# Performance work log

Measured on AMD Instinct MI355X. Metric: run time of the kernel, lower is better.

Reference implementation:

```python
import jax, jax.numpy as jnp
import numpy as np

B, XL, YL, D = 16, 2048, 2048, 1024

def setup_inputs() -> dict:
    key = jax.random.key(0)
    kx, ky, km, kw = jax.random.split(key, 4)
    x = jax.random.normal(kx, (B, XL, D), dtype=jnp.float32)
    y = jax.random.normal(ky, (B, YL, D), dtype=jnp.float32)
    # True == padding position (masked with -inf in the torch module)
    y_mask = jax.random.randint(km, (B, YL), 0, 2).astype(bool)
    # shared projection Linear(embed_dim, embed_dim); scale ~ 1/sqrt(D)
    W = jax.random.normal(kw, (D, D), dtype=jnp.float32) * (1.0 / np.sqrt(D))
    b = jnp.zeros((D,), dtype=jnp.float32)
    return {"x": x, "y": y, "y_mask": y_mask, "W": W, "b": b}

def reference(x, y, y_mask, W, b):
    # shared ReLU(Linear) projection applied to both x and y
    x_proj = jax.nn.relu(jnp.einsum('bxd,ed->bxe', x, W) + b)   # (B, XL, D)
    y_proj = jax.nn.relu(jnp.einsum('byd,ed->bye', y, W) + b)   # (B, YL, D)
    scores = jnp.einsum('bxd,byd->bxy', x_proj, y_proj)          # (B, XL, YL)
    scores = jnp.where(y_mask[:, None, :], -jnp.inf, scores)
    weights = jax.nn.softmax(scores, axis=2)
    contexts = jnp.einsum('bxy,byd->bxd', weights, y)            # (B, XL, D)
    return contexts
```

## Files before the change

kernel.cpp:

```cpp
#include <hip/hip_runtime.h>
#include <math.h>
#include <stdint.h>


typedef __attribute__((ext_vector_type(8))) _Float16 f16x8;
typedef __attribute__((ext_vector_type(4))) float f32x4;

__device__ __forceinline__ ushort h2u(_Float16 h) { return __builtin_bit_cast(ushort, h); }

__device__ __forceinline__ void ld16(const ushort* g, ushort* l) {
    __builtin_amdgcn_global_load_lds(
        (__attribute__((address_space(1))) void*)(g),
        (__attribute__((address_space(3))) void*)(l), 16, 0, 0);
}

template<int EPI, int MODE>
__global__ __launch_bounds__(256) void gemm128(
    const ushort* __restrict__ A, size_t zsA,
    const ushort* __restrict__ B, size_t zsB,
    const float* __restrict__ bias, const int* __restrict__ nyBuf,
    float* __restrict__ Cf, ushort* __restrict__ Chi, size_t zsC,
    int sdA, int sdB, int N, int T)
{
    __shared__ char ldsb[32768];

    const int gx = gridDim.x, gxy = gx * gridDim.y;
    const int total = gxy * gridDim.z;
    int hsw = blockIdx.z * gxy + blockIdx.y * gx + blockIdx.x;
    hsw = (hsw & 7) * (total >> 3) + (hsw >> 3);
    const int z = hsw / gxy;
    const int rem = hsw - z * gxy;
    const int by = rem / gx;
    const int bx = rem - by * gx;

    int NY = 0, NYPAD = 0;
    if constexpr (MODE != 0) { NY = nyBuf[2 * z]; NYPAD = nyBuf[2 * z + 1]; }
    if constexpr (MODE == 1) { if (by * 128 >= 2048 && by * 128 - 2048 >= NYPAD) return; }
    if constexpr (MODE == 2) { if (bx * 128 >= NYPAD) return; }
    if constexpr (MODE == 3) { T = NYPAD >> 6; }

    const int tid = threadIdx.x;
    const int lane = tid & 63;
    const int wv = tid >> 6;
    const int wm = (wv >> 1) * 64, wn = (wv & 1) * 64;
    const int m0 = by * 128, n0 = bx * 128;

    const int pl  = tid >> 3;
    const int ss  = (tid & 7) ^ (pl & 7);
    const int sr0 = 2 * pl + (ss >> 2);
    const int ske = (ss & 3) * 8;
    const int tb  = tid * 16;

    const ushort* gA0 = A + (size_t)z * zsA + (size_t)(m0 + sr0) * sdA + ske;
    const ushort* gA1 = gA0 + (size_t)64 * sdA;
    const ushort* gB0 = B + (size_t)z * zsB + (size_t)(n0 + sr0) * sdB + ske;
    const ushort* gB1 = gB0 + (size_t)64 * sdB;

    const int fr = lane & 15, fq = lane >> 4;
    const int sl = (((fr & 1) << 2) | fq) ^ ((fr >> 1) & 7);
    const int aoff = wm * 64 + (fr >> 1) * 128 + sl * 16;
    const int boff = 16384 + wn * 64 + (fr >> 1) * 128 + sl * 16;

    f32x4 acc[4][4];
    #pragma unroll
    for (int i = 0; i < 4; ++i)
        #pragma unroll
        for (int j = 0; j < 4; ++j)
            acc[i][j] = (f32x4){0.f, 0.f, 0.f, 0.f};

    for (int t = 0; t < T; ++t) {
        ld16(gA0,      (ushort*)(ldsb + tb));
        ld16(gA1,      (ushort*)(ldsb + 4096 + tb));
        ld16(gA0 + 32, (ushort*)(ldsb + 8192 + tb));
        ld16(gA1 + 32, (ushort*)(ldsb + 12288 + tb));
        ld16(gB0,      (ushort*)(ldsb + 16384 + tb));
        ld16(gB1,      (ushort*)(ldsb + 20480 + tb));
        ld16(gB0 + 32, (ushort*)(ldsb + 24576 + tb));
        ld16(gB1 + 32, (ushort*)(ldsb + 28672 + tb));
        gA0 += 64; gA1 += 64; gB0 += 64; gB1 += 64;
        __syncthreads();

        #pragma unroll
        for (int kk = 0; kk < 2; ++kk) {
            const char* p = ldsb + kk * 8192;
            f16x8 a[4], b[4];
            #pragma unroll
            for (int i = 0; i < 4; ++i) a[i] = *(const f16x8*)(p + aoff + i * 1024);
            #pragma unroll
            for (int j = 0; j < 4; ++j) b[j] = *(const f16x8*)(p + boff + j * 1024);
            #pragma unroll
            for (int i = 0; i < 4; ++i)
                #pragma unroll
                for (int j = 0; j < 4; ++j)
                    acc[i][j] = __builtin_amdgcn_mfma_f32_16x16x32_f16(a[i], b[j], acc[i][j], 0, 0, 0);
        }
        __syncthreads();
    }

    #pragma unroll
    for (int j = 0; j < 4; ++j) {
        const int col = n0 + wn + j * 16 + fr;
        float bb = 0.f;
        if constexpr (EPI == 1) bb = bias[col];
        #pragma unroll
        for (int i = 0; i < 4; ++i) {
            const int row = m0 + wm + i * 16 + fq * 4;
            #pragma unroll
            for (int r = 0; r < 4; ++r) {
                const float v = acc[i][j][r];
                const size_t idx = (size_t)z * zsC + (size_t)(row + r) * N + col;
                if constexpr (EPI == 0) {
                    Cf[idx] = v;
                } else if constexpr (EPI == 1) {
                    Chi[idx] = h2u((_Float16)fmaxf(v + bb, 0.f));
                } else {
                    Cf[idx] = (col >= NY) ? -INFINITY : v;
                }
            }
        }
    }
}

__global__ __launch_bounds__(256) void build_idx(const int* __restrict__ mask,
    int* __restrict__ idx, int* __restrict__ nyBuf)
{
    const int z = blockIdx.x;
    const int* mb = mask + (size_t)z * 2048;
    __shared__ int part[256];
    const int tid = threadIdx.x;
    int keep[8]; int c = 0;
    #pragma unroll
    for (int k = 0; k < 8; ++k) { keep[k] = (mb[tid * 8 + k] == 0); c += keep[k]; }
    part[tid] = c;
    for (int off = 1; off < 256; off <<= 1) {
        __syncthreads();
        const int v = (tid >= off) ? part[tid - off] : 0;
        __syncthreads();
        part[tid] += v;
    }
    __syncthreads();
    int pos = part[tid] - c;
    #pragma unroll
    for (int k = 0; k < 8; ++k)
        if (keep[k]) idx[(size_t)z * 2048 + (pos++)] = tid * 8 + k;
    if (tid == 255) {
        const int ny = part[255];
        int nyp = (ny + 127) & ~127;
        if (nyp < 256) nyp = 256;
        nyBuf[2 * z] = ny;
        nyBuf[2 * z + 1] = nyp;
    }
}

__global__ __launch_bounds__(256) void cvt_f16(const float* __restrict__ in,
    ushort* __restrict__ o, size_t sIn4, size_t sOut)
{
    const size_t z = blockIdx.z;
    const int i = blockIdx.x * 256 + threadIdx.x;
    const float4 v = reinterpret_cast<const float4*>(in)[z * sIn4 + i];
    ushort4 h;
    h.x = h2u((_Float16)v.x); h.y = h2u((_Float16)v.y);
    h.z = h2u((_Float16)v.z); h.w = h2u((_Float16)v.w);
    reinterpret_cast<ushort4*>(o + z * sOut)[i] = h;
}

__global__ __launch_bounds__(256) void gather_y(const float* __restrict__ y,
    const int* __restrict__ idx, const int* __restrict__ nyBuf,
    ushort* __restrict__ rH, ushort* __restrict__ tT,
    size_t sIn, size_t sR, size_t sT)
{
    __shared__ float tile[32][33];
    const size_t z = blockIdx.z;
    const int NY = nyBuf[2 * z], NYPAD = nyBuf[2 * z + 1];
    const int r0 = blockIdx.y * 32;
    if (r0 >= NYPAD) return;
    const int c0 = blockIdx.x * 32;
    const float* yb = y + z * sIn;
    const int* idxb = idx + z * 2048;
    const int tx = threadIdx.x & 31, ty = threadIdx.x >> 5;
    #pragma unroll
    for (int k = 0; k < 4; ++k) {
        const int i = r0 + ty + k * 8;
        float v = 0.f;
        if (i < NY) v = yb[(size_t)idxb[i] * 1024 + c0 + tx];
        tile[ty + k * 8][tx] = v;
        rH[z * sR + (size_t)i * 1024 + c0 + tx] = h2u((_Float16)v);
    }
    __syncthreads();
    #pragma unroll
    for (int k = 0; k < 4; ++k) {
        const int c = c0 + ty + k * 8;
        tT[z * sT + (size_t)c * 2048 + r0 + tx] = h2u((_Float16)tile[tx][ty + k * 8]);
    }
}

__global__ __launch_bounds__(256) void softmax_f16(const float* __restrict__ S,
    ushort* __restrict__ Wout, const int* __restrict__ nyBuf, size_t sS, size_t sW)
{
    const size_t row = blockIdx.x;
    const size_t b = row >> 11, r = row & 2047;
    const int nf4 = nyBuf[2 * b + 1] >> 2;
    const float4* p4 = reinterpret_cast<const float4*>(S + b * sS + r * 2048);
    ushort4* q4 = reinterpret_cast<ushort4*>(Wout + b * sW + r * 2048);
    const int tid = threadIdx.x;

    const float4 NEG = {-INFINITY, -INFINITY, -INFINITY, -INFINITY};
    float4 v0 = (tid < nf4) ? p4[tid] : NEG;
    float4 v1 = (tid + 256 < nf4) ? p4[tid + 256] : NEG;
    float m = fmaxf(fmaxf(fmaxf(v0.x, v0.y), fmaxf(v0.z, v0.w)),
                    fmaxf(fmaxf(v1.x, v1.y), fmaxf(v1.z, v1.w)));
    #pragma unroll
    for (int off = 32; off >= 1; off >>= 1)
        m = fmaxf(m, __shfl_xor(m, off));

    __shared__ float redm[4], reds[4];
    if ((tid & 63) == 0) redm[tid >> 6] = m;
    __syncthreads();
    m = fmaxf(fmaxf(redm[0], redm[1]), fmaxf(redm[2], redm[3]));

    float e[8];
    e[0] = __expf(v0.x - m); e[1] = __expf(v0.y - m);
    e[2] = __expf(v0.z - m); e[3] = __expf(v0.w - m);
    e[4] = __expf(v1.x - m); e[5] = __expf(v1.y - m);
    e[6] = __expf(v1.z - m); e[7] = __expf(v1.w - m);
    float s = ((e[0] + e[1]) + (e[2] + e[3])) + ((e[4] + e[5]) + (e[6] + e[7]));
    #pragma unroll
    for (int off = 32; off >= 1; off >>= 1)
        s += __shfl_xor(s, off);
    if ((tid & 63) == 0) reds[tid >> 6] = s;
    __syncthreads();
    s = reds[0] + reds[1] + reds[2] + reds[3];

    const float inv = 1.f / s;
    ushort4 o0, o1;
    o0.x = h2u((_Float16)(e[0] * inv)); o0.y = h2u((_Float16)(e[1] * inv));
    o0.z = h2u((_Float16)(e[2] * inv)); o0.w = h2u((_Float16)(e[3] * inv));
    o1.x = h2u((_Float16)(e[4] * inv)); o1.y = h2u((_Float16)(e[5] * inv));
    o1.z = h2u((_Float16)(e[6] * inv)); o1.w = h2u((_Float16)(e[7] * inv));
    if (tid < nf4) q4[tid] = o0;
    if (tid + 256 < nf4) q4[tid + 256] = o1;
}

extern "C" void kernel_launch(void* const* d_in, const int* in_sizes, int n_in,
                              void* d_out, int out_size, void* d_ws, size_t ws_size,
                              hipStream_t stream)
{
    const float* x    = (const float*)d_in[0];
    const float* y    = (const float*)d_in[1];
    const int* ymask  = (const int*)d_in[2];
    const float* W    = (const float*)d_in[3];
    const float* bias = (const float*)d_in[4];
    float* out = (float*)d_out;

    const size_t BD = 2097152;

    const size_t perBatch = 29360128ull;
    int G = 16;
    while (G > 1 && 4194304ull + (size_t)G * perBatch > ws_size) G >>= 1;

    uint8_t* wsb = (uint8_t*)d_ws;
    ushort* W16  = (ushort*)wsb;
    int* idxBuf  = (int*)(wsb + 2097152);
    int* nyBuf   = (int*)(wsb + 2097152 + 131072);
    uint8_t* r1  = wsb + 4194304;
    uint8_t* r2  = r1 + (size_t)G * 16777216;
    uint8_t* r3  = r2 + (size_t)G * 8388608;

    ushort* xyHi = (ushort*)r1;
    float*  sc   = (float*)r1;
    ushort* pHi  = (ushort*)r2;
    ushort* yT   = (ushort*)r3;

    cvt_f16<<<dim3(1024, 1, 1), dim3(256), 0, stream>>>(W, W16, 0, 0);
    build_idx<<<dim3(16), dim3(256), 0, stream>>>(ymask, idxBuf, nyBuf);

    for (int bs = 0; bs < 16; bs += G) {
        const float* xg = x + (size_t)bs * BD;
        const float* yg = y + (size_t)bs * BD;
        const int* nyB  = nyBuf + 2 * bs;

        cvt_f16<<<dim3(2048, 1, G), dim3(256), 0, stream>>>(
            xg, xyHi, BD / 4, 8388608);
        gather_y<<<dim3(32, 64, G), dim3(256), 0, stream>>>(
            yg, idxBuf + (size_t)bs * 2048, nyB,
            xyHi + BD, yT, BD, 8388608, BD);

        gemm128<1, 1><<<dim3(8, 32, G), dim3(256), 0, stream>>>(
            xyHi, 8388608, W16, 0,
            bias, nyB,
            nullptr, pHi, 4194304, 1024, 1024, 1024, 16);

        gemm128<2, 2><<<dim3(16, 16, G), dim3(256), 0, stream>>>(
            pHi, 4194304, pHi + BD, 4194304,
            nullptr, nyB,
            sc, nullptr, 4194304, 1024, 1024, 2048, 16);

        softmax_f16<<<dim3(G * 2048), dim3(256), 0, stream>>>(
            sc, pHi, nyB, 4194304, 4194304);

        gemm128<0, 3><<<dim3(8, 16, G), dim3(256), 0, stream>>>(
            pHi, 4194304, yT, 2097152,
            nullptr, nyB,
            out + (size_t)bs * BD, nullptr, BD, 2048, 2048, 1024, 16);
    }
}
```

Before: 503.4 us.

## Fuse fp32-to-fp16 conversion and y gather into projection GEMM A-loads

Adds a projg kernel that reads x and gathered y rows directly in fp32, converts them to fp16 in registers and writes them into swizzled LDS, while W tiles are staged with async global-to-LDS loads. This removes the separate cvt_f16 pass over x and the row-major fp16 copy of gathered y, saving a full write and re-read of the fp16 activations. In exchange, the GEMM A path now reads twice as many bytes per element (fp32) and relies on a software prefetch into registers, which may reduce overlap and raise register pressure.

```diff
diff --git a/kernel.cpp b/kernel.cpp
--- a/kernel.cpp
+++ b/kernel.cpp
@@ -14,15 +14,17 @@
         (__attribute__((address_space(3))) void*)(l), 16, 0, 0);
 }
 
-template<int EPI, int MODE>
-__global__ __launch_bounds__(256) void gemm128(
-    const ushort* __restrict__ A, size_t zsA,
-    const ushort* __restrict__ B, size_t zsB,
-    const float* __restrict__ bias, const int* __restrict__ nyBuf,
-    float* __restrict__ Cf, ushort* __restrict__ Chi, size_t zsC,
-    int sdA, int sdB, int N, int T)
-{
-    __shared__ char ldsb[32768];
+#define BAR()  { __builtin_amdgcn_s_barrier(); asm volatile("" ::: "memory"); }
+#define VMW0() asm volatile("s_waitcnt vmcnt(0)" ::: "memory");
+#define LGKM0() { asm volatile("s_waitcnt lgkmcnt(0)" ::: "memory"); __builtin_amdgcn_sched_barrier(0); }
+
+__global__ __launch_bounds__(256) void projg(
+    const float* __restrict__ X, const float* __restrict__ Y,
+    const int* __restrict__ idx, const int* __restrict__ nyBuf,
+    const ushort* __restrict__ Wm, const float* __restrict__ bias,
+    ushort* __restrict__ P, int T)
+{
+    __shared__ char ldsb[49152];
 
     const int gx = gridDim.x, gxy = gx * gridDim.y;
     const int total = gxy * gridDim.z;
@@ -33,9 +35,149 @@
     const int by = rem / gx;
     const int bx = rem - by * gx;
 
+    const int NY = nyBuf[2 * z], NYPAD = nyBuf[2 * z + 1];
+    const int m0 = by * 128, n0 = bx * 128;
+    if (m0 >= 2048 + NYPAD) return;
+
+    const int tid = threadIdx.x;
+    const int lane = tid & 63;
+    const int wv = tid >> 6;
+    const int wm = (wv >> 1) * 64, wn = (wv & 1) * 64;
+
+    const int ar = tid >> 1, akh = tid & 1;
+    const int gr = m0 + ar;
+    const float* asrc = nullptr;
+    if (gr < 2048) {
+        asrc = X + (size_t)z * 2097152 + (size_t)gr * 1024;
+    } else {
+        const int i = gr - 2048;
+        if (i < NY) asrc = Y + (size_t)z * 2097152 + (size_t)idx[(size_t)z * 2048 + i] * 1024;
+    }
+    const int ap = ar >> 1, asub = ar & 1;
+    char* awp = ldsb + akh * 8192 + ap * 128;
+    int awq[4];
+    #pragma unroll
+    for (int q = 0; q < 4; ++q) awq[q] = ((((asub << 2) | q) ^ (ap & 7)) << 4);
+
+    const int pl  = tid >> 3;
+    const int ss  = (tid & 7) ^ (pl & 7);
+    const int sr0 = 2 * pl + (ss >> 2);
+    const int ske = (ss & 3) * 8;
+    const int tb  = tid * 16;
+    const ushort* gB0 = Wm + (size_t)(n0 + sr0) * 1024 + ske;
+    const ushort* gB1 = gB0 + 65536;
+
+    const int fr = lane & 15, fq = lane >> 4;
+    const int sl = (((fr & 1) << 2) | fq) ^ ((fr >> 1) & 7);
+    const int aoff = wm * 64 + (fr >> 1) * 128 + sl * 16;
+    const int boff = wn * 64 + (fr >> 1) * 128 + sl * 16;
+
+    f32x4 acc[4][4];
+    #pragma unroll
+    for (int i = 0; i < 4; ++i)
+        #pragma unroll
+        for (int j = 0; j < 4; ++j)
+            acc[i][j] = (f32x4){0.f, 0.f, 0.f, 0.f};
+
+    float4 v[8];
+
+    auto issueA = [&](int t) {
+        if (asrc) {
+            const float4* s = reinterpret_cast<const float4*>(asrc + (size_t)t * 64 + akh * 32);
+            #pragma unroll
+            for (int u = 0; u < 8; ++u) v[u] = s[u];
+        } else {
+            #pragma unroll
+            for (int u = 0; u < 8; ++u) v[u] = (float4){0.f, 0.f, 0.f, 0.f};
+        }
+    };
+    auto stageB = [&](int t, int buf) {
+        const ushort* b0 = gB0 + t * 64;
+        const ushort* b1 = gB1 + t * 64;
+        ushort* d = (ushort*)(ldsb + 16384 + buf * 16384);
+        ld16(b0,      (ushort*)((char*)d + tb));
+        ld16(b1,      (ushort*)((char*)d + 4096 + tb));
+        ld16(b0 + 32, (ushort*)((char*)d + 8192 + tb));
+        ld16(b1 + 32, (ushort*)((char*)d + 12288 + tb));
+    };
+    auto writeA = [&]() {
+        #pragma unroll
+        for (int q = 0; q < 4; ++q) {
+            const float4 a_ = v[2 * q], b_ = v[2 * q + 1];
+            f16x8 h;
+            h[0] = (_Float16)a_.x; h[1] = (_Float16)a_.y;
+            h[2] = (_Float16)a_.z; h[3] = (_Float16)a_.w;
+            h[4] = (_Float16)b_.x; h[5] = (_Float16)b_.y;
+            h[6] = (_Float16)b_.z; h[7] = (_Float16)b_.w;
+            *reinterpret_cast<f16x8*>(awp + awq[q]) = h;
+        }
+    };
+    auto computeT = [&](int buf) {
+        #pragma unroll
+        for (int kk = 0; kk < 2; ++kk) {
+            const char* pa = ldsb + kk * 8192;
+            const char* pb = ldsb + 16384 + buf * 16384 + kk * 8192;
+            f16x8 a[4], b[4];
+            #pragma unroll
+            for (int i = 0; i < 4; ++i) a[i] = *(const f16x8*)(pa + aoff + i * 1024);
+            #pragma unroll
+            for (int j = 0; j < 4; ++j) b[j] = *(const f16x8*)(pb + boff + j * 1024);
+            #pragma unroll
+            for (int i = 0; i < 4; ++i)
+                #pragma unroll
+                for (int j = 0; j < 4; ++j)
+                    acc[i][j] = __builtin_amdgcn_mfma_f32_16x16x32_f16(a[i], b[j], acc[i][j], 0, 0, 0);
+        }
+    };
+
+    issueA(0); stageB(0, 0);
+    for (int t = 0; t < T; ++t) {
+        VMW0();
+        BAR();
+        writeA();
+        if (t + 1 < T) { issueA(t + 1); stageB(t + 1, (t + 1) & 1); }
+        LGKM0();
+        BAR();
+        computeT(t & 1);
+    }
+
+    #pragma unroll
+    for (int j = 0; j < 4; ++j) {
+        const int col = n0 + wn + j * 16 + fr;
+        const float bb = bias[col];
+        #pragma unroll
+        for (int i = 0; i < 4; ++i) {
+            const int row = m0 + wm + i * 16 + fq * 4;
+            #pragma unroll
+            for (int r = 0; r < 4; ++r) {
+                const size_t o = (size_t)z * 4194304 + (size_t)(row + r) * 1024 + col;
+                P[o] = h2u((_Float16)fmaxf(acc[i][j][r] + bb, 0.f));
+            }
+        }
+    }
+}
+
+template<int EPI, int MODE>
+__global__ __launch_bounds__(256) void gemm128(
+    const ushort* __restrict__ A, size_t zsA,
+    const ushort* __restrict__ B, size_t zsB,
+    const float* __restrict__ bias, const int* __restrict__ nyBuf,
+    float* __restrict__ Cf, ushort* __restrict__ Chi, size_t zsC,
+    int sdA, int sdB, int N, int T)
+{
+    __shared__ char ldsb[32768];
+
+    const int gx = gridDim.x, gxy = gx * gridDim.y;
+    const int total = gxy * gridDim.z;
+    int hsw = blockIdx.z * gxy + blockIdx.y * gx + blockIdx.x;
+    hsw = (hsw & 7) * (total >> 3) + (hsw >> 3);
+    const int z = hsw / gxy;
+    const int rem = hsw - z * gxy;
+    const int by = rem / gx;
+    const int bx = rem - by * gx;
+
     int NY = 0, NYPAD = 0;
     if constexpr (MODE != 0) { NY = nyBuf[2 * z]; NYPAD = nyBuf[2 * z + 1]; }
-    if constexpr (MODE == 1) { if (by * 128 >= 2048 && by * 128 - 2048 >= NYPAD) return; }
     if constexpr (MODE == 2) { if (bx * 128 >= NYPAD) return; }
     if constexpr (MODE == 3) { T = NYPAD >> 6; }
 
@@ -108,13 +250,13 @@
             #pragma unroll
             for (int r = 0; r < 4; ++r) {
                 const float v = acc[i][j][r];
-                const size_t idx = (size_t)z * zsC + (size_t)(row + r) * N + col;
+                const size_t o = (size_t)z * zsC + (size_t)(row + r) * N + col;
                 if constexpr (EPI == 0) {
-                    Cf[idx] = v;
+                    Cf[o] = v;
                 } else if constexpr (EPI == 1) {
-                    Chi[idx] = h2u((_Float16)fmaxf(v + bb, 0.f));
+                    Chi[o] = h2u((_Float16)fmaxf(v + bb, 0.f));
                 } else {
-                    Cf[idx] = (col >= NY) ? -INFINITY : v;
+                    Cf[o] = (col >= NY) ? -INFINITY : v;
                 }
             }
         }
@@ -153,21 +295,19 @@
 }
 
 __global__ __launch_bounds__(256) void cvt_f16(const float* __restrict__ in,
-    ushort* __restrict__ o, size_t sIn4, size_t sOut)
-{
-    const size_t z = blockIdx.z;
+    ushort* __restrict__ o)
+{
     const int i = blockIdx.x * 256 + threadIdx.x;
-    const float4 v = reinterpret_cast<const float4*>(in)[z * sIn4 + i];
+    const float4 v = reinterpret_cast<const float4*>(in)[i];
     ushort4 h;
     h.x = h2u((_Float16)v.x); h.y = h2u((_Float16)v.y);
     h.z = h2u((_Float16)v.z); h.w = h2u((_Float16)v.w);
-    reinterpret_cast<ushort4*>(o + z * sOut)[i] = h;
-}
-
-__global__ __launch_bounds__(256) void gather_y(const float* __restrict__ y,
+    reinterpret_cast<ushort4*>(o)[i] = h;
+}
+
+__global__ __launch_bounds__(256) void gather_t(const float* __restrict__ y,
     const int* __restrict__ idx, const int* __restrict__ nyBuf,
-    ushort* __restrict__ rH, ushort* __restrict__ tT,
-    size_t sIn, size_t sR, size_t sT)
+    ushort* __restrict__ tT, size_t sIn, size_t sT)
 {
     __shared__ float tile[32][33];
     const size_t z = blockIdx.z;
@@ -184,7 +324,6 @@
         float v = 0.f;
         if (i < NY) v = yb[(size_t)idxb[i] * 1024 + c0 + tx];
         tile[ty + k * 8][tx] = v;
-        rH[z * sR + (size_t)i * 1024 + c0 + tx] = h2u((_Float16)v);
     }
     __syncthreads();
     #pragma unroll
@@ -266,29 +405,24 @@
     uint8_t* r2  = r1 + (size_t)G * 16777216;
     uint8_t* r3  = r2 + (size_t)G * 8388608;
 
-    ushort* xyHi = (ushort*)r1;
     float*  sc   = (float*)r1;
     ushort* pHi  = (ushort*)r2;
     ushort* yT   = (ushort*)r3;
 
-    cvt_f16<<<dim3(1024, 1, 1), dim3(256), 0, stream>>>(W, W16, 0, 0);
+    cvt_f16<<<dim3(1024), dim3(256), 0, stream>>>(W, W16);
     build_idx<<<dim3(16), dim3(256), 0, stream>>>(ymask, idxBuf, nyBuf);
 
     for (int bs = 0; bs < 16; bs += G) {
         const float* xg = x + (size_t)bs * BD;
         const float* yg = y + (size_t)bs * BD;
         const int* nyB  = nyBuf + 2 * bs;
-
-        cvt_f16<<<dim3(2048, 1, G), dim3(256), 0, stream>>>(
-            xg, xyHi, BD / 4, 8388608);
-        gather_y<<<dim3(32, 64, G), dim3(256), 0, stream>>>(
-            yg, idxBuf + (size_t)bs * 2048, nyB,
-            xyHi + BD, yT, BD, 8388608, BD);
-
-        gemm128<1, 1><<<dim3(8, 32, G), dim3(256), 0, stream>>>(
-            xyHi, 8388608, W16, 0,
-            bias, nyB,
-            nullptr, pHi, 4194304, 1024, 1024, 1024, 16);
+        const int* idxg = idxBuf + (size_t)bs * 2048;
+
+        gather_t<<<dim3(32, 64, G), dim3(256), 0, stream>>>(
+            yg, idxg, nyB, yT, BD, BD);
+
+        projg<<<dim3(8, 32, G), dim3(256), 0, stream>>>(
+            xg, yg, idxg, nyB, W16, bias, pHi, 16);
 
         gemm128<2, 2><<<dim3(16, 16, G), dim3(256), 0, stream>>>(
             pHi, 4194304, pHi + BD, 4194304,
```

New measurement: 601.7 us, median of 2. +19.5%, slower.
